# Performance work log

Hardware: AMD Instinct MI355X
Metric: run time of the kernel (lower is better)

## Reference

```python
import jax, jax.numpy as jnp
import numpy as np

NP_, NG_ = 20000, 5000            # protein / go_annotation node counts
D_FEAT, D_HID, N_CLS = 512, 128, 1000
E_PP, E_PG, E_GP = 240000, 100000, 100000
NEG_SLOPE = -0.2                  # note: the repo default slope is negative
EPS = 1e-12


def _l2norm(x):
    n = jnp.linalg.norm(x, axis=1, keepdims=True)
    return x / jnp.maximum(n, EPS)


def _edge_softmax(logits, dst, n):
    # per-destination-node softmax over incoming edges, per feature channel
    m = jax.ops.segment_max(logits, dst, num_segments=n)
    e = jnp.exp(logits - m[dst])
    s = jax.ops.segment_sum(e, dst, num_segments=n)
    return e / s[dst]


def _type_attn(h_src, h_dst, src, dst, Wl, bl, Wr, br):
    # GCN-normalized aggregation onto dst nodes, then type-level attention logits,
    # broadcast back to edges (copy_u on the reversed relation graph).
    ns, nd = h_src.shape[0], h_dst.shape[0]
    ones = jnp.ones(src.shape[0], dtype=h_src.dtype)
    outdeg = jnp.clip(jax.ops.segment_sum(ones, src, num_segments=ns), 1.0)
    feat = h_src * (outdeg ** -0.5)[:, None]
    rst = jax.ops.segment_sum(feat[src], dst, num_segments=nd)
    indeg = jnp.clip(jax.ops.segment_sum(ones, dst, num_segments=nd), 1.0)
    rst = rst * (indeg ** -0.5)[:, None]
    ea = jax.nn.elu((h_dst @ Wl + bl) + (rst @ Wr + br))  # [nd, D_HID]
    return ea[dst]                                        # [E, D_HID]


def setup_inputs() -> dict:
    key = jax.random.key(0)
    ks = iter(jax.random.split(key, 40))

    def nrm(shape, s=0.05):
        return jax.random.normal(next(ks), shape, dtype=jnp.float32) * s

    def ri(n, hi):
        return jax.random.randint(next(ks), (n,), 0, hi, dtype=jnp.int32)

    zeros = lambda n: jnp.zeros((n,), jnp.float32)
    return dict(
        x_protein=jax.random.normal(next(ks), (NP_, D_FEAT), dtype=jnp.float32),
        x_go=jax.random.normal(next(ks), (NG_, N_CLS), dtype=jnp.float32),
        src_pp=ri(E_PP, NP_), dst_pp=ri(E_PP, NP_),
        src_pg=ri(E_PG, NP_), dst_pg=ri(E_PG, NG_),
        src_gp=ri(E_GP, NG_), dst_gp=ri(E_GP, NP_),
        W1p=nrm((D_FEAT, D_HID)), b1p=zeros(D_HID),
        W1g=nrm((N_CLS, D_HID)), b1g=zeros(D_HID),
        Wl_p=nrm((D_HID, D_HID)), bl_p=zeros(D_HID),
        Wl_g=nrm((D_HID, D_HID)), bl_g=zeros(D_HID),
        Wr_p=nrm((D_HID, D_HID)), br_p=zeros(D_HID),
        Wr_g=nrm((D_HID, D_HID)), br_g=zeros(D_HID),
        Wnl=nrm((D_HID, D_HID)), bnl=zeros(D_HID),
        Wnr=nrm((D_HID, D_HID)), bnr=zeros(D_HID),
        Wfc=nrm((D_HID, N_CLS)), bfc=zeros(N_CLS),
    )


def reference(x_protein, x_go, src_pp, dst_pp, src_pg, dst_pg, src_gp, dst_gp,
              W1p, b1p, W1g, b1g, Wl_p, bl_p, Wl_g, bl_g,
              Wr_p, br_p, Wr_g, br_g, Wnl, bnl, Wnr, bnr, Wfc, bfc):
    # input projection + row-wise l2 norm (dropout disabled / eval mode)
    hp = _l2norm(x_protein @ W1p + b1p)   # [NP, D_HID]
    hg = _l2norm(x_go @ W1g + b1g)        # [NG, D_HID]

    # ---- TypeAttention over each canonical etype ----
    a_pp = _type_attn(hp, hp, src_pp, dst_pp, Wl_p, bl_p, Wr_p, br_p)
    a_pg = _type_attn(hp, hg, src_pg, dst_pg, Wl_g, bl_g, Wr_p, br_p)
    a_gp = _type_attn(hg, hp, src_gp, dst_gp, Wl_p, bl_p, Wr_g, br_g)

    # homogeneous view: proteins [0,NP), go_annotation [NP,NP+NG)
    gsrc = jnp.concatenate([src_pp, src_pg, src_gp + NP_])
    gdst = jnp.concatenate([dst_pp, dst_pg + NP_, dst_gp])
    alpha = jnp.concatenate([a_pp, a_pg, a_gp], axis=0)   # [E, D_HID]
    n = NP_ + NG_
    alpha = _edge_softmax(alpha, gdst, n)

    # ---- NodeAttention on the homogeneous graph ----
    x = jnp.concatenate([hp, hg], axis=0)                 # [N, D_HID]
    hl = (x @ Wnl + bnl)[gsrc]
    hr = (x @ Wnr + bnr)[gdst]
    e = (hl + hr) * alpha
    e = jnp.where(e > 0, e, NEG_SLOPE * e)                # LeakyReLU(slope=-0.2)
    a = _edge_softmax(e, gdst, n)
    h = jax.ops.segment_sum(x[gsrc] * a, gdst, num_segments=n)

    out = h @ Wfc + bfc   # [N, N_CLS]; rows [:NP]=protein, [NP:]=go_annotation
    return out
```

## Files before the change

kernel.cpp:

```cpp
#include <hip/hip_runtime.h>
#include <math.h>

#define NP 20000
#define NG 5000
#define NTOT 25000
#define DF 512
#define NCLS 1000
#define DH 128
#define EPP 240000
#define EPG 100000
#define EGP 100000
#define ETOT 440000
#define FS 16
#define HB 16

typedef __attribute__((ext_vector_type(8))) __bf16 bf16x8;
typedef __attribute__((ext_vector_type(4))) float f32x4;

__device__ __forceinline__ void gl2lds16(const void* g, void* l) {
    __builtin_amdgcn_global_load_lds(
        (const __attribute__((address_space(1))) unsigned int*)g,
        (__attribute__((address_space(3))) unsigned int*)l, 16, 0, 0);
}

__device__ __forceinline__ float b2f(unsigned short u) {
    union { unsigned int i; float f; } c; c.i = ((unsigned int)u) << 16; return c.f;
}

__global__ __launch_bounds__(1024) void hist_part_kernel(
    const int* __restrict__ src_pp, const int* __restrict__ dst_pp,
    const int* __restrict__ src_pg, const int* __restrict__ dst_pg,
    const int* __restrict__ src_gp, const int* __restrict__ dst_gp,
    int* __restrict__ partial)
{
    __shared__ int bins[20000];
    const int job = blockIdx.y, b = blockIdx.x;
    const int* idx; int nbins, nedge; size_t pbase;
    switch (job) {
    case 0: idx = src_pp; nbins = 20000; nedge = EPP; pbase = 0;       break;
    case 1: idx = dst_pp; nbins = 20000; nedge = EPP; pbase = 320000;  break;
    case 2: idx = src_pg; nbins = 20000; nedge = EPG; pbase = 640000;  break;
    case 3: idx = dst_pg; nbins = 5000;  nedge = EPG; pbase = 960000;  break;
    case 4: idx = src_gp; nbins = 5000;  nedge = EGP; pbase = 1040000; break;
    default: idx = dst_gp; nbins = 20000; nedge = EGP; pbase = 1120000; break;
    }
    for (int i = threadIdx.x; i < nbins; i += 1024) bins[i] = 0;
    __syncthreads();
    const int chunk = (nedge + HB - 1) / HB;
    const int e0 = b * chunk, e1 = min(e0 + chunk, nedge);
    for (int e = e0 + threadIdx.x; e < e1; e += 1024) atomicAdd(&bins[idx[e]], 1);
    __syncthreads();
    int* dst = partial + pbase + (size_t)b * nbins;
    for (int i = threadIdx.x; i < nbins; i += 1024) dst[i] = bins[i];
}

__global__ __launch_bounds__(256) void hist_merge_kernel(const int* __restrict__ partial,
    int* __restrict__ outdeg_pp, int* __restrict__ indeg_pp,
    int* __restrict__ outdeg_pg, int* __restrict__ indeg_pg,
    int* __restrict__ outdeg_gp, int* __restrict__ indeg_gp)
{
    const int job = blockIdx.y;
    const int nbins = (job == 3 || job == 4) ? 5000 : 20000;
    const int bin = blockIdx.x * 256 + threadIdx.x;
    if (bin >= nbins) return;
    size_t pbase;
    int* outp;
    switch (job) {
    case 0: pbase = 0;       outp = outdeg_pp; break;
    case 1: pbase = 320000;  outp = indeg_pp;  break;
    case 2: pbase = 640000;  outp = outdeg_pg; break;
    case 3: pbase = 960000;  outp = indeg_pg;  break;
    case 4: pbase = 1040000; outp = outdeg_gp; break;
    default: pbase = 1120000; outp = indeg_gp; break;
    }
    const int* p = partial + pbase + bin;
    int s = 0;
#pragma unroll
    for (int b = 0; b < HB; b++) s += p[(size_t)b * nbins];
    outp[bin] = s;
}

__global__ __launch_bounds__(1024) void scan_kernel(const int* __restrict__ indeg_pp,
                                                    const int* __restrict__ indeg_gp,
                                                    const int* __restrict__ indeg_pg,
                                                    int* __restrict__ row_ptr)
{
    __shared__ int part[1024];
    int t = threadIdx.x;
    const int CH = (NTOT + 1023) / 1024;
    int base = t * CH;
    auto cntf = [&](int idx) -> int {
        return (idx < NP) ? (indeg_pp[idx] + indeg_gp[idx]) : indeg_pg[idx - NP];
    };
    int s = 0;
    for (int i = 0; i < CH; i++) { int idx = base + i; if (idx < NTOT) s += cntf(idx); }
    part[t] = s;
    __syncthreads();
    for (int off = 1; off < 1024; off <<= 1) {
        int v = (t >= off) ? part[t - off] : 0;
        __syncthreads();
        part[t] += v;
        __syncthreads();
    }
    int run = (t == 0) ? 0 : part[t - 1];
    for (int i = 0; i < CH; i++) {
        int idx = base + i;
        if (idx < NTOT) { row_ptr[idx] = run; run += cntf(idx); }
    }
    if (t == 1023) row_ptr[NTOT] = part[1023];
}

__global__ void scatter_kernel(const int* __restrict__ src_pp, const int* __restrict__ dst_pp,
                               const int* __restrict__ src_pg, const int* __restrict__ dst_pg,
                               const int* __restrict__ src_gp, const int* __restrict__ dst_gp,
                               const int* __restrict__ outdeg_pp, const int* __restrict__ outdeg_pg,
                               const int* __restrict__ outdeg_gp,
                               const int* __restrict__ row_ptr, int* fill,
                               int2* __restrict__ edata)
{
    int e = blockIdx.x * blockDim.x + threadIdx.x;
    int s, d, t; float sc;
    if (e < EPP) {
        s = src_pp[e]; d = dst_pp[e]; t = 0;
        sc = rsqrtf((float)max(outdeg_pp[s], 1));
    } else if (e < EPP + EPG) {
        int i = e - EPP; s = src_pg[i]; d = NP + dst_pg[i]; t = 1;
        sc = rsqrtf((float)max(outdeg_pg[s], 1));
    } else if (e < ETOT) {
        int i = e - EPP - EPG; int sl = src_gp[i]; s = NP + sl; d = dst_gp[i]; t = 2;
        sc = rsqrtf((float)max(outdeg_gp[sl], 1));
    } else return;
    int pos = row_ptr[d] + atomicAdd(&fill[d * FS], 1);
    edata[pos] = make_int2(s | (t << 16), __float_as_int(sc));
}

__global__ __launch_bounds__(256) void conv_x_kernel(const float* __restrict__ xp, const float* __restrict__ xg,
                                                     __bf16* __restrict__ xpb, __bf16* __restrict__ xgb)
{
    long long e = ((long long)blockIdx.x * 256 + threadIdx.x) * 8;
    __bf16 pk[8];
    if (blockIdx.y == 0) {
        if (e >= (long long)20032 * 512) return;
        int row = (int)(e >> 9), k = (int)(e & 511);
        if (row < NP) {
            f32x4 v0 = *(const f32x4*)(xp + (size_t)row * 512 + k);
            f32x4 v1 = *(const f32x4*)(xp + (size_t)row * 512 + k + 4);
#pragma unroll
            for (int i = 0; i < 4; i++) { pk[i] = (__bf16)v0[i]; pk[4 + i] = (__bf16)v1[i]; }
        } else {
#pragma unroll
            for (int i = 0; i < 8; i++) pk[i] = (__bf16)0.f;
        }
        *(bf16x8*)(xpb + e) = *(bf16x8*)pk;
    } else {
        if (e >= (long long)5056 * 1024) return;
        int row = (int)(e >> 10), k = (int)(e & 1023);
        if (row < NG && k + 7 < 1000) {
            f32x4 v0 = *(const f32x4*)(xg + (size_t)row * 1000 + k);
            f32x4 v1 = *(const f32x4*)(xg + (size_t)row * 1000 + k + 4);
#pragma unroll
            for (int i = 0; i < 4; i++) { pk[i] = (__bf16)v0[i]; pk[4 + i] = (__bf16)v1[i]; }
        } else {
#pragma unroll
            for (int i = 0; i < 8; i++) {
                int kk = k + i;
                pk[i] = (__bf16)((row < NG && kk < 1000) ? xg[(size_t)row * 1000 + kk] : 0.f);
            }
        }
        *(bf16x8*)(xgb + e) = *(bf16x8*)pk;
    }
}

__global__ __launch_bounds__(256) void conv_w_kernel(
    const float* W1p, const float* W1g, const float* Wlp, const float* Wrp, const float* Wrg,
    const float* Wnl, const float* Wnr, const float* Wfc,
    __bf16* w1pt, __bf16* w1gt, __bf16* wlpt, __bf16* wrpt, __bf16* wrgt,
    __bf16* wnlt, __bf16* wnrt, __bf16* wfct)
{
    int e = blockIdx.x * 256 + threadIdx.x;
    switch (blockIdx.y) {
    case 0: if (e < 128 * 512)  { int n = e >> 9, k = e & 511;  w1pt[e] = (__bf16)W1p[(size_t)k * 128 + n]; } break;
    case 1: if (e < 128 * 1024) { int n = e >> 10, k = e & 1023; w1gt[e] = (__bf16)(k < 1000 ? W1g[(size_t)k * 128 + n] : 0.f); } break;
    case 2: if (e < 16384) { int n = e >> 7, k = e & 127; wlpt[e] = (__bf16)Wlp[(size_t)k * 128 + n]; } break;
    case 3: if (e < 16384) { int n = e >> 7, k = e & 127; wrpt[e] = (__bf16)Wrp[(size_t)k * 128 + n]; } break;
    case 4: if (e < 16384) { int n = e >> 7, k = e & 127; wrgt[e] = (__bf16)Wrg[(size_t)k * 128 + n]; } break;
    case 5: if (e < 16384) { int n = e >> 7, k = e & 127; wnlt[e] = (__bf16)Wnl[(size_t)k * 128 + n]; } break;
    case 6: if (e < 16384) { int n = e >> 7, k = e & 127; wnrt[e] = (__bf16)Wnr[(size_t)k * 128 + n]; } break;
    case 7: if (e < 1024 * 128) { int n = e >> 7, k = e & 127; wfct[e] = (__bf16)(n < 1000 ? Wfc[(size_t)k * 1000 + n] : 0.f); } break;
    }
}

struct GJob {
    const __bf16* A1; const __bf16* A2;
    const __bf16* B1; const __bf16* B2;
    const float* b1; const float* b2;
    float* O1; float* O2; __bf16* Ob;
    int M, N, Kp, ksteps;
};

template<int ACT, int DUALA, int DUALW, int EMIT>
__global__ __launch_bounds__(256) void gemm_bt(GJob j0, GJob j1, int split)
{
    __shared__ __align__(16) __bf16 As[64 * 32];
    __shared__ __align__(16) __bf16 A2s[DUALA ? 64 * 32 : 8];
    __shared__ __align__(16) __bf16 Bs[128 * 32];
    __shared__ __align__(16) __bf16 B2s[(DUALA || DUALW) ? 128 * 32 : 8];
    __shared__ float part[2][64];

    GJob j; int bx;
    if ((int)blockIdx.x < split) { j = j0; bx = blockIdx.x; }
    else { j = j1; bx = blockIdx.x - split; }

    const int tid = threadIdx.x;
    const int wave = tid >> 6, lane = tid & 63;
    const int wr = wave >> 1, wc = wave & 1;
    const int l15 = lane & 15, lh = lane >> 4;
    const int row0 = bx * 64;
    const int col0 = blockIdx.y * 128;

    const size_t aoff = (size_t)(row0 + (tid >> 2)) * j.Kp + (tid & 3) * 8;
    const size_t boff0 = (size_t)(col0 + (tid >> 2)) * j.Kp + (tid & 3) * 8;
    const size_t boff1 = boff0 + (size_t)64 * j.Kp;
    char* alds  = (char*)As + wave * 1024;
    char* a2lds = (char*)A2s + wave * 1024;
    char* blds0 = (char*)Bs + wave * 1024;
    char* blds1 = (char*)Bs + 4096 + wave * 1024;
    char* b2lds0 = (char*)B2s + wave * 1024;
    char* b2lds1 = (char*)B2s + 4096 + wave * 1024;

    f32x4 acc[2][4], acc2[2][4];
#pragma unroll
    for (int fm = 0; fm < 2; fm++)
#pragma unroll
        for (int fn = 0; fn < 4; fn++) {
            acc[fm][fn] = (f32x4)0.f;
            if (DUALW) acc2[fm][fn] = (f32x4)0.f;
        }

    for (int ks = 0; ks < j.ksteps; ks++) {
        const int k0 = ks * 32;
        __syncthreads();
        gl2lds16(j.A1 + aoff + k0, alds);
        if (DUALA) gl2lds16(j.A2 + aoff + k0, a2lds);
        gl2lds16(j.B1 + boff0 + k0, blds0);
        gl2lds16(j.B1 + boff1 + k0, blds1);
        if (DUALA || DUALW) {
            gl2lds16(j.B2 + boff0 + k0, b2lds0);
            gl2lds16(j.B2 + boff1 + k0, b2lds1);
        }
        __syncthreads();

#pragma unroll
        for (int fm = 0; fm < 2; fm++) {
            bf16x8 a = *(const bf16x8*)&As[(wr * 32 + fm * 16 + l15) * 32 + lh * 8];
            bf16x8 a2;
            if (DUALA) a2 = *(const bf16x8*)&A2s[(wr * 32 + fm * 16 + l15) * 32 + lh * 8];
#pragma unroll
            for (int fn = 0; fn < 4; fn++) {
                bf16x8 b = *(const bf16x8*)&Bs[(wc * 64 + fn * 16 + l15) * 32 + lh * 8];
                acc[fm][fn] = __builtin_amdgcn_mfma_f32_16x16x32_bf16(a, b, acc[fm][fn], 0, 0, 0);
                if (DUALA) {
                    bf16x8 b2 = *(const bf16x8*)&B2s[(wc * 64 + fn * 16 + l15) * 32 + lh * 8];
                    acc[fm][fn] = __builtin_amdgcn_mfma_f32_16x16x32_bf16(a2, b2, acc[fm][fn], 0, 0, 0);
                }
                if (DUALW) {
                    bf16x8 b2 = *(const bf16x8*)&B2s[(wc * 64 + fn * 16 + l15) * 32 + lh * 8];
                    acc2[fm][fn] = __builtin_amdgcn_mfma_f32_16x16x32_bf16(a, b2, acc2[fm][fn], 0, 0, 0);
                }
            }
        }
    }

    float bias[4], bias2[4];
#pragma unroll
    for (int fn = 0; fn < 4; fn++) {
        int col = col0 + wc * 64 + fn * 16 + l15;
        bias[fn] = 0.f; bias2[fn] = 0.f;
        if (col < j.N) {
            bias[fn] = DUALA ? (j.b1[col] + j.b2[col]) : j.b1[col];
            if (DUALW) bias2[fn] = j.b2[col];
        }
    }

    float vv[2][4][4];
#pragma unroll
    for (int fm = 0; fm < 2; fm++)
#pragma unroll
        for (int fn = 0; fn < 4; fn++)
#pragma unroll
            for (int r = 0; r < 4; r++) {
                float v = acc[fm][fn][r] + bias[fn];
                if (ACT == 1) v = v > 0.f ? v : (expf(v) - 1.f);
                vv[fm][fn][r] = v;
            }

    float scale[2][4];
#pragma unroll
    for (int fm = 0; fm < 2; fm++)
#pragma unroll
        for (int r = 0; r < 4; r++) scale[fm][r] = 1.f;

    if (ACT == 2) {
        float s[2][4];
#pragma unroll
        for (int fm = 0; fm < 2; fm++)
#pragma unroll
            for (int r = 0; r < 4; r++) {
                float v = 0.f;
#pragma unroll
                for (int fn = 0; fn < 4; fn++) v += vv[fm][fn][r] * vv[fm][fn][r];
                v += __shfl_xor(v, 1);
                v += __shfl_xor(v, 2);
                v += __shfl_xor(v, 4);
                v += __shfl_xor(v, 8);
                s[fm][r] = v;
            }
        __syncthreads();
        if (l15 == 0) {
#pragma unroll
            for (int fm = 0; fm < 2; fm++)
#pragma unroll
                for (int r = 0; r < 4; r++)
                    part[wc][wr * 32 + fm * 16 + lh * 4 + r] = s[fm][r];
        }
        __syncthreads();
#pragma unroll
        for (int fm = 0; fm < 2; fm++)
#pragma unroll
            for (int r = 0; r < 4; r++) {
                int rl = wr * 32 + fm * 16 + lh * 4 + r;
                float ss = part[0][rl] + part[1][rl];
                scale[fm][r] = 1.f / fmaxf(sqrtf(ss), 1e-12f);
            }
    }

#pragma unroll
    for (int fm = 0; fm < 2; fm++)
#pragma unroll
        for (int fn = 0; fn < 4; fn++)
#pragma unroll
            for (int r = 0; r < 4; r++) {
                int row = row0 + wr * 32 + fm * 16 + lh * 4 + r;
                int col = col0 + wc * 64 + fn * 16 + l15;
                if (row < j.M && col < j.N) {
                    float v = vv[fm][fn][r] * scale[fm][r];
                    if (EMIT != 2) j.O1[(size_t)row * j.N + col] = v;
                    if (EMIT != 0) j.Ob[(size_t)row * j.N + col] = (__bf16)v;
                    if (DUALW) j.O2[(size_t)row * j.N + col] = acc2[fm][fn][r] + bias2[fn];
                }
            }
}

__global__ __launch_bounds__(128) void rst_agg_kernel(const __bf16* __restrict__ x,
                                                      const int* __restrict__ row_ptr,
                                                      const int2* __restrict__ edata,
                                                      const int* __restrict__ indeg_pp,
                                                      const int* __restrict__ indeg_gp,
                                                      __bf16* __restrict__ rppb, __bf16* __restrict__ rgpb)
{
    int d = blockIdx.x;
    int c = threadIdx.x;
    int beg = row_ptr[d], end = row_ptr[d + 1];
    float spp = 0.f, sgp = 0.f;
    __shared__ int pl[128];
    __shared__ float sc[128];
    const unsigned short* xu = (const unsigned short*)x;
    for (int base = beg; base < end; base += 128) {
        int n = min(128, end - base);
        __syncthreads();
        if (c < n) { int2 e2 = edata[base + c]; pl[c] = e2.x; sc[c] = __int_as_float(e2.y); }
        __syncthreads();
        for (int i = 0; i < n; i++) {
            int p = pl[i]; int s = p & 0xFFFF; int t = p >> 16;
            float v = b2f(xu[(size_t)s * DH + c]) * sc[i];
            if (t == 0) spp += v; else sgp += v;
        }
    }
    float ipp = rsqrtf((float)max(indeg_pp[d], 1));
    float igp = rsqrtf((float)max(indeg_gp[d], 1));
    rppb[(size_t)d * DH + c] = (__bf16)(spp * ipp);
    rgpb[(size_t)d * DH + c] = (__bf16)(sgp * igp);
}

__global__ void wa_kernel(const int* __restrict__ indeg_pp, const int* __restrict__ indeg_gp,
                          float* __restrict__ eapp, float* __restrict__ eagp)
{
    int idx = blockIdx.x * blockDim.x + threadIdx.x;
    if (idx >= NP * DH) return;
    int d = idx >> 7;
    int npp = indeg_pp[d], ngp = indeg_gp[d];
    float app = eapp[idx], agp = eagp[idx];
    float wpp = 0.f, wgp = 0.f;
    if (npp > 0 && ngp > 0) {
        float mx = fmaxf(app, agp);
        float epp = __expf(app - mx), egp = __expf(agp - mx);
        float den = (float)npp * epp + (float)ngp * egp;
        wpp = epp / den; wgp = egp / den;
    } else if (npp > 0) wpp = 1.f / (float)npp;
    else if (ngp > 0) wgp = 1.f / (float)ngp;
    eapp[idx] = wpp;
    eagp[idx] = wgp;
}

__global__ __launch_bounds__(128) void node_attn_kernel(const __bf16* __restrict__ x,
                                                        const __bf16* __restrict__ hlb,
                                                        const float* __restrict__ hr,
                                                        const float* __restrict__ wpp_arr, const float* __restrict__ wgp_arr,
                                                        const int* __restrict__ indeg_pg,
                                                        const int* __restrict__ row_ptr, const int2* __restrict__ edata,
                                                        __bf16* __restrict__ hb)
{
    int d = blockIdx.x, c = threadIdx.x;
    int beg = row_ptr[d], end = row_ptr[d + 1];
    float hrd = hr[(size_t)d * DH + c];
    float wpp = 0.f, wgp = 0.f;
    if (d < NP) {
        wpp = wpp_arr[(size_t)d * DH + c];
        wgp = wgp_arr[(size_t)d * DH + c];
    } else {
        float wpg = 1.f / (float)max(indeg_pg[d - NP], 1);
        wpp = wpg; wgp = wpg;
    }
    float ssum = 0.f, acc = 0.f;
    __shared__ int pl[128];
    const unsigned short* xu = (const unsigned short*)x;
    const unsigned short* hu = (const unsigned short*)hlb;
    for (int base = beg; base < end; base += 128) {
        int n = min(128, end - base);
        __syncthreads();
        if (c < n) pl[c] = edata[base + c].x;
        __syncthreads();
        for (int i = 0; i < n; i++) {
            int p = pl[i]; int s = p & 0xFFFF; int t = p >> 16;
            float al = (t == 0) ? wpp : wgp;
            float e = (b2f(hu[(size_t)s * DH + c]) + hrd) * al;
            e = fmaxf(e, -0.2f * e);
            float pw = __expf(e);
            float xv = b2f(xu[(size_t)s * DH + c]);
            ssum += pw;
            acc += pw * xv;
        }
    }
    hb[(size_t)d * DH + c] = (__bf16)((end > beg) ? acc / ssum : 0.f);
}

extern "C" void kernel_launch(void* const* d_in, const int* in_sizes, int n_in,
                              void* d_out, int out_size, void* d_ws, size_t ws_size,
                              hipStream_t stream)
{
    const float* x_protein = (const float*)d_in[0];
    const float* x_go      = (const float*)d_in[1];
    const int* src_pp = (const int*)d_in[2];
    const int* dst_pp = (const int*)d_in[3];
    const int* src_pg = (const int*)d_in[4];
    const int* dst_pg = (const int*)d_in[5];
    const int* src_gp = (const int*)d_in[6];
    const int* dst_gp = (const int*)d_in[7];
    const float* W1p = (const float*)d_in[8];
    const float* b1p = (const float*)d_in[9];
    const float* W1g = (const float*)d_in[10];
    const float* b1g = (const float*)d_in[11];
    const float* Wl_p = (const float*)d_in[12];
    const float* bl_p = (const float*)d_in[13];
    const float* Wr_p = (const float*)d_in[16];
    const float* br_p = (const float*)d_in[17];
    const float* Wr_g = (const float*)d_in[18];
    const float* br_g = (const float*)d_in[19];
    const float* Wnl = (const float*)d_in[20];
    const float* bnl = (const float*)d_in[21];
    const float* Wnr = (const float*)d_in[22];
    const float* bnr = (const float*)d_in[23];
    const float* Wfc = (const float*)d_in[24];
    const float* bfc = (const float*)d_in[25];
    float* out = (float*)d_out;

    size_t off = 0;
    char* base = (char*)d_ws;
    auto alloc = [&](size_t words) { void* p = base + off * 4; off += (words + 7) & ~(size_t)7; return p; };

    __bf16* xb   = (__bf16*)alloc((size_t)25024 * 128 / 2);
    float*  hr   = (float*)alloc((size_t)25000 * 128);
    __bf16* hlb  = (__bf16*)alloc((size_t)25024 * 128 / 2);
    __bf16* rppb = (__bf16*)alloc((size_t)20032 * 128 / 2);
    __bf16* rgpb = (__bf16*)alloc((size_t)20032 * 128 / 2);
    char* R1 = (char*)alloc((size_t)5128192 + 2588672);
    int*    partial = (int*)R1;
    __bf16* xpb = (__bf16*)R1;
    __bf16* xgb = (__bf16*)(R1 + (size_t)20032 * 512 * 2);
    float*  wpp = (float*)R1;
    float*  wgp = wpp + (size_t)20000 * 128;
    __bf16* haggb = (__bf16*)(wgp + (size_t)20000 * 128);
    __bf16* w1pt = (__bf16*)alloc(128 * 512 / 2);
    __bf16* w1gt = (__bf16*)alloc(128 * 1024 / 2);
    __bf16* wlpt = (__bf16*)alloc(128 * 128 / 2);
    __bf16* wrpt = (__bf16*)alloc(128 * 128 / 2);
    __bf16* wrgt = (__bf16*)alloc(128 * 128 / 2);
    __bf16* wnlt = (__bf16*)alloc(128 * 128 / 2);
    __bf16* wnrt = (__bf16*)alloc(128 * 128 / 2);
    __bf16* wfct = (__bf16*)alloc(1024 * 128 / 2);
    int* outdeg_pp = (int*)alloc(NP);
    int* outdeg_pg = (int*)alloc(NP);
    int* outdeg_gp = (int*)alloc(NG);
    int* indeg_pp  = (int*)alloc(NP);
    int* indeg_gp  = (int*)alloc(NP);
    int* indeg_pg  = (int*)alloc(NG);
    int* fill      = (int*)alloc((size_t)NTOT * FS);
    int* row_ptr   = (int*)alloc(NTOT + 1);
    int2* edata    = (int2*)alloc((size_t)ETOT * 2);

    hipMemsetAsync(fill, 0, (size_t)NTOT * FS * sizeof(int), stream);

    hist_part_kernel<<<dim3(HB, 6), 1024, 0, stream>>>(
        src_pp, dst_pp, src_pg, dst_pg, src_gp, dst_gp, partial);
    hist_merge_kernel<<<dim3((20000 + 255) / 256, 6), 256, 0, stream>>>(
        partial, outdeg_pp, indeg_pp, outdeg_pg, indeg_pg, outdeg_gp, indeg_gp);
    scan_kernel<<<1, 1024, 0, stream>>>(indeg_pp, indeg_gp, indeg_pg, row_ptr);
    scatter_kernel<<<(ETOT + 255) / 256, 256, 0, stream>>>(
        src_pp, dst_pp, src_pg, dst_pg, src_gp, dst_gp,
        outdeg_pp, outdeg_pg, outdeg_gp, row_ptr, fill, edata);

    conv_x_kernel<<<dim3(5008, 2), 256, 0, stream>>>(x_protein, x_go, xpb, xgb);
    conv_w_kernel<<<dim3(512, 8), 256, 0, stream>>>(W1p, W1g, Wl_p, Wr_p, Wr_g, Wnl, Wnr, Wfc,
                                                    w1pt, w1gt, wlpt, wrpt, wrgt, wnlt, wnrt, wfct);

    {
        GJob p0 = { xpb, nullptr, w1pt, nullptr, b1p, nullptr, nullptr, nullptr, xb, NP, 128, 512, 16 };
        GJob p1 = { xgb, nullptr, w1gt, nullptr, b1g, nullptr, nullptr, nullptr,
                    xb + (size_t)NP * 128, NG, 128, 1024, 32 };
        gemm_bt<2, 0, 0, 2><<<392, 256, 0, stream>>>(p0, p1, 313);
    }

    rst_agg_kernel<<<NP, 128, 0, stream>>>(xb, row_ptr, edata, indeg_pp, indeg_gp, rppb, rgpb);

    {
        GJob e0 = { xb, rppb, wlpt, wrpt, bl_p, br_p, wpp, nullptr, nullptr, NP, 128, 128, 4 };
        GJob e1 = { xb, rgpb, wlpt, wrgt, bl_p, br_g, wgp, nullptr, nullptr, NP, 128, 128, 4 };
        gemm_bt<1, 1, 0, 0><<<626, 256, 0, stream>>>(e0, e1, 313);
    }

    wa_kernel<<<(NP * DH + 255) / 256, 256, 0, stream>>>(indeg_pp, indeg_gp, wpp, wgp);

    {
        GJob h0 = { xb, nullptr, wnlt, wnrt, bnl, bnr, nullptr, hr, hlb, NTOT, 128, 128, 4 };
        gemm_bt<0, 0, 1, 2><<<391, 256, 0, stream>>>(h0, h0, 1 << 30);
    }

    node_attn_kernel<<<NTOT, 128, 0, stream>>>(xb, hlb, hr, wpp, wgp, indeg_pg, row_ptr, edata, haggb);

    {
        GJob o0 = { haggb, nullptr, wfct, nullptr, bfc, nullptr, out, nullptr, nullptr, NTOT, NCLS, 128, 4 };
        gemm_bt<0, 0, 0, 0><<<dim3(391, 8), 256, 0, stream>>>(o0, o0, 1 << 30);
    }

    (void)in_sizes; (void)n_in; (void)out_size; (void)ws_size;
}
```

Before: 264.3 us.

## Fuse fp32 protein conversion into GEMM, merge type-attn GEMM with softmax, interleave x/hl

The protein feature matrix is now loaded in fp32 straight into the projection GEMM and converted to bf16 in registers, so the separate conversion pass and its bf16 buffer go away. The two type-attention GEMMs and the weight-softmax kernel become one kernel that computes the three products and the ELU and softmax in its epilogue. x and hl are stored interleaved so node attention reads both with one 32-bit load, and hr is now stored in bf16. Both gather kernels move to 256 threads, with the edges split between two halves and combined through LDS. In exchange, hr loses precision and the fp32 A tile doubles the LDS traffic of the projection GEMM.

```diff
diff --git a/kernel.cpp b/kernel.cpp
--- a/kernel.cpp
+++ b/kernel.cpp
@@ -11,7 +11,7 @@
 #define EPG 100000
 #define EGP 100000
 #define ETOT 440000
-#define FS 16
+#define FS 8
 #define HB 16
 
 typedef __attribute__((ext_vector_type(8))) __bf16 bf16x8;
@@ -63,8 +63,7 @@
     const int nbins = (job == 3 || job == 4) ? 5000 : 20000;
     const int bin = blockIdx.x * 256 + threadIdx.x;
     if (bin >= nbins) return;
-    size_t pbase;
-    int* outp;
+    size_t pbase; int* outp;
     switch (job) {
     case 0: pbase = 0;       outp = outdeg_pp; break;
     case 1: pbase = 320000;  outp = indeg_pp;  break;
@@ -134,41 +133,25 @@
     edata[pos] = make_int2(s | (t << 16), __float_as_int(sc));
 }
 
-__global__ __launch_bounds__(256) void conv_x_kernel(const float* __restrict__ xp, const float* __restrict__ xg,
-                                                     __bf16* __restrict__ xpb, __bf16* __restrict__ xgb)
+__global__ __launch_bounds__(256) void conv_xg_kernel(const float* __restrict__ xg, __bf16* __restrict__ xgb)
 {
     long long e = ((long long)blockIdx.x * 256 + threadIdx.x) * 8;
+    if (e >= (long long)5056 * 1024) return;
+    int row = (int)(e >> 10), k = (int)(e & 1023);
     __bf16 pk[8];
-    if (blockIdx.y == 0) {
-        if (e >= (long long)20032 * 512) return;
-        int row = (int)(e >> 9), k = (int)(e & 511);
-        if (row < NP) {
-            f32x4 v0 = *(const f32x4*)(xp + (size_t)row * 512 + k);
-            f32x4 v1 = *(const f32x4*)(xp + (size_t)row * 512 + k + 4);
-#pragma unroll
-            for (int i = 0; i < 4; i++) { pk[i] = (__bf16)v0[i]; pk[4 + i] = (__bf16)v1[i]; }
-        } else {
-#pragma unroll
-            for (int i = 0; i < 8; i++) pk[i] = (__bf16)0.f;
-        }
-        *(bf16x8*)(xpb + e) = *(bf16x8*)pk;
+    if (row < NG && k + 7 < 1000) {
+        f32x4 v0 = *(const f32x4*)(xg + (size_t)row * 1000 + k);
+        f32x4 v1 = *(const f32x4*)(xg + (size_t)row * 1000 + k + 4);
+#pragma unroll
+        for (int i = 0; i < 4; i++) { pk[i] = (__bf16)v0[i]; pk[4 + i] = (__bf16)v1[i]; }
     } else {
-        if (e >= (long long)5056 * 1024) return;
-        int row = (int)(e >> 10), k = (int)(e & 1023);
-        if (row < NG && k + 7 < 1000) {
-            f32x4 v0 = *(const f32x4*)(xg + (size_t)row * 1000 + k);
-            f32x4 v1 = *(const f32x4*)(xg + (size_t)row * 1000 + k + 4);
-#pragma unroll
-            for (int i = 0; i < 4; i++) { pk[i] = (__bf16)v0[i]; pk[4 + i] = (__bf16)v1[i]; }
-        } else {
-#pragma unroll
-            for (int i = 0; i < 8; i++) {
-                int kk = k + i;
-                pk[i] = (__bf16)((row < NG && kk < 1000) ? xg[(size_t)row * 1000 + kk] : 0.f);
-            }
-        }
-        *(bf16x8*)(xgb + e) = *(bf16x8*)pk;
-    }
+#pragma unroll
+        for (int i = 0; i < 8; i++) {
+            int kk = k + i;
+            pk[i] = (__bf16)((row < NG && kk < 1000) ? xg[(size_t)row * 1000 + kk] : 0.f);
+        }
+    }
+    *(bf16x8*)(xgb + e) = *(bf16x8*)pk;
 }
 
 __global__ __launch_bounds__(256) void conv_w_kernel(
@@ -191,40 +174,41 @@
 }
 
 struct GJob {
-    const __bf16* A1; const __bf16* A2;
-    const __bf16* B1; const __bf16* B2;
+    const void* A1; const __bf16* B1; const __bf16* B2;
     const float* b1; const float* b2;
-    float* O1; float* O2; __bf16* Ob;
+    float* O1; void* O2; __bf16* Ob; __bf16* Oi;
     int M, N, Kp, ksteps;
 };
 
-template<int ACT, int DUALA, int DUALW, int EMIT>
-__global__ __launch_bounds__(256) void gemm_bt(GJob j0, GJob j1, int split)
-{
-    __shared__ __align__(16) __bf16 As[64 * 32];
-    __shared__ __align__(16) __bf16 A2s[DUALA ? 64 * 32 : 8];
+template<int ACT, int DUALW, int EMIT, int AF32>
+__global__ __launch_bounds__(256) void gemm_bt(GJob j)
+{
+    __shared__ __align__(16) __bf16 As[AF32 ? 8 : 64 * 32];
+    __shared__ __align__(16) float Asf[AF32 ? 64 * 32 : 4];
     __shared__ __align__(16) __bf16 Bs[128 * 32];
-    __shared__ __align__(16) __bf16 B2s[(DUALA || DUALW) ? 128 * 32 : 8];
+    __shared__ __align__(16) __bf16 B2s[DUALW ? 128 * 32 : 8];
     __shared__ float part[2][64];
-
-    GJob j; int bx;
-    if ((int)blockIdx.x < split) { j = j0; bx = blockIdx.x; }
-    else { j = j1; bx = blockIdx.x - split; }
 
     const int tid = threadIdx.x;
     const int wave = tid >> 6, lane = tid & 63;
     const int wr = wave >> 1, wc = wave & 1;
     const int l15 = lane & 15, lh = lane >> 4;
-    const int row0 = bx * 64;
+    const int row0 = blockIdx.x * 64;
     const int col0 = blockIdx.y * 128;
 
+    const __bf16* A1b = (const __bf16*)j.A1;
+    const float*  A1f = (const float*)j.A1;
+
     const size_t aoff = (size_t)(row0 + (tid >> 2)) * j.Kp + (tid & 3) * 8;
+    const size_t a0off = (size_t)min(row0 + (tid >> 3), j.M - 1) * j.Kp + (tid & 7) * 4;
+    const size_t a1off = (size_t)min(row0 + 32 + (tid >> 3), j.M - 1) * j.Kp + (tid & 7) * 4;
     const size_t boff0 = (size_t)(col0 + (tid >> 2)) * j.Kp + (tid & 3) * 8;
     const size_t boff1 = boff0 + (size_t)64 * j.Kp;
-    char* alds  = (char*)As + wave * 1024;
-    char* a2lds = (char*)A2s + wave * 1024;
-    char* blds0 = (char*)Bs + wave * 1024;
-    char* blds1 = (char*)Bs + 4096 + wave * 1024;
+    char* alds   = (char*)As + wave * 1024;
+    char* aldsf0 = (char*)Asf + wave * 1024;
+    char* aldsf1 = (char*)Asf + 4096 + wave * 1024;
+    char* blds0  = (char*)Bs + wave * 1024;
+    char* blds1  = (char*)Bs + 4096 + wave * 1024;
     char* b2lds0 = (char*)B2s + wave * 1024;
     char* b2lds1 = (char*)B2s + 4096 + wave * 1024;
 
@@ -240,11 +224,15 @@
     for (int ks = 0; ks < j.ksteps; ks++) {
         const int k0 = ks * 32;
         __syncthreads();
-        gl2lds16(j.A1 + aoff + k0, alds);
-        if (DUALA) gl2lds16(j.A2 + aoff + k0, a2lds);
+        if constexpr (AF32) {
+            gl2lds16(A1f + a0off + k0, aldsf0);
+            gl2lds16(A1f + a1off + k0, aldsf1);
+        } else {
+            gl2lds16(A1b + aoff + k0, alds);
+        }
         gl2lds16(j.B1 + boff0 + k0, blds0);
         gl2lds16(j.B1 + boff1 + k0, blds1);
-        if (DUALA || DUALW) {
+        if constexpr (DUALW) {
             gl2lds16(j.B2 + boff0 + k0, b2lds0);
             gl2lds16(j.B2 + boff1 + k0, b2lds1);
         }
@@ -252,18 +240,23 @@
 
 #pragma unroll
         for (int fm = 0; fm < 2; fm++) {
-            bf16x8 a = *(const bf16x8*)&As[(wr * 32 + fm * 16 + l15) * 32 + lh * 8];
-            bf16x8 a2;
-            if (DUALA) a2 = *(const bf16x8*)&A2s[(wr * 32 + fm * 16 + l15) * 32 + lh * 8];
+            bf16x8 a;
+            if constexpr (AF32) {
+                const float* ap = &Asf[(wr * 32 + fm * 16 + l15) * 32 + lh * 8];
+                f32x4 a0 = *(const f32x4*)ap;
+                f32x4 a1 = *(const f32x4*)(ap + 4);
+                __bf16 pk[8];
+#pragma unroll
+                for (int i = 0; i < 4; i++) { pk[i] = (__bf16)a0[i]; pk[4 + i] = (__bf16)a1[i]; }
+                a = *(bf16x8*)pk;
+            } else {
+                a = *(const bf16x8*)&As[(wr * 32 + fm * 16 + l15) * 32 + lh * 8];
+            }
 #pragma unroll
             for (int fn = 0; fn < 4; fn++) {
                 bf16x8 b = *(const bf16x8*)&Bs[(wc * 64 + fn * 16 + l15) * 32 + lh * 8];
                 acc[fm][fn] = __builtin_amdgcn_mfma_f32_16x16x32_bf16(a, b, acc[fm][fn], 0, 0, 0);
-                if (DUALA) {
-                    bf16x8 b2 = *(const bf16x8*)&B2s[(wc * 64 + fn * 16 + l15) * 32 + lh * 8];
-                    acc[fm][fn] = __builtin_amdgcn_mfma_f32_16x16x32_bf16(a2, b2, acc[fm][fn], 0, 0, 0);
-                }
-                if (DUALW) {
+                if constexpr (DUALW) {
                     bf16x8 b2 = *(const bf16x8*)&B2s[(wc * 64 + fn * 16 + l15) * 32 + lh * 8];
                     acc2[fm][fn] = __builtin_amdgcn_mfma_f32_16x16x32_bf16(a, b2, acc2[fm][fn], 0, 0, 0);
                 }
@@ -277,7 +270,7 @@
         int col = col0 + wc * 64 + fn * 16 + l15;
         bias[fn] = 0.f; bias2[fn] = 0.f;
         if (col < j.N) {
-            bias[fn] = DUALA ? (j.b1[col] + j.b2[col]) : j.b1[col];
+            bias[fn] = j.b1[col];
             if (DUALW) bias2[fn] = j.b2[col];
         }
     }
@@ -288,11 +281,7 @@
 #pragma unroll
         for (int fn = 0; fn < 4; fn++)
 #pragma unroll
-            for (int r = 0; r < 4; r++) {
-                float v = acc[fm][fn][r] + bias[fn];
-                if (ACT == 1) v = v > 0.f ? v : (expf(v) - 1.f);
-                vv[fm][fn][r] = v;
-            }
+            for (int r = 0; r < 4; r++) vv[fm][fn][r] = acc[fm][fn][r] + bias[fn];
 
     float scale[2][4];
 #pragma unroll
@@ -300,7 +289,7 @@
 #pragma unroll
         for (int r = 0; r < 4; r++) scale[fm][r] = 1.f;
 
-    if (ACT == 2) {
+    if constexpr (ACT == 2) {
         float s[2][4];
 #pragma unroll
         for (int fm = 0; fm < 2; fm++)
@@ -344,14 +333,122 @@
                 int col = col0 + wc * 64 + fn * 16 + l15;
                 if (row < j.M && col < j.N) {
                     float v = vv[fm][fn][r] * scale[fm][r];
-                    if (EMIT != 2) j.O1[(size_t)row * j.N + col] = v;
-                    if (EMIT != 0) j.Ob[(size_t)row * j.N + col] = (__bf16)v;
-                    if (DUALW) j.O2[(size_t)row * j.N + col] = acc2[fm][fn][r] + bias2[fn];
+                    if constexpr (EMIT == 0) j.O1[(size_t)row * j.N + col] = v;
+                    if constexpr (EMIT == 2) j.Ob[(size_t)row * j.N + col] = (__bf16)v;
+                    if constexpr (EMIT == 3) {
+                        j.Ob[(size_t)row * j.N + col] = (__bf16)v;
+                        j.Oi[(size_t)row * 256 + col * 2] = (__bf16)v;
+                    }
+                    if constexpr (EMIT == 4) j.Oi[(size_t)row * 256 + col * 2 + 1] = (__bf16)v;
+                    if constexpr (DUALW)
+                        ((__bf16*)j.O2)[(size_t)row * j.N + col] = (__bf16)(acc2[fm][fn][r] + bias2[fn]);
                 }
             }
 }
 
-__global__ __launch_bounds__(128) void rst_agg_kernel(const __bf16* __restrict__ x,
+__global__ __launch_bounds__(256) void ea_wa_kernel(
+    const __bf16* __restrict__ xb, const __bf16* __restrict__ rppb, const __bf16* __restrict__ rgpb,
+    const __bf16* __restrict__ wl, const __bf16* __restrict__ wrp, const __bf16* __restrict__ wrg,
+    const float* __restrict__ blp, const float* __restrict__ brp, const float* __restrict__ brg,
+    const int* __restrict__ indeg_pp, const int* __restrict__ indeg_gp,
+    float* __restrict__ wpp, float* __restrict__ wgp)
+{
+    __shared__ __align__(16) __bf16 A1s[64 * 32], A2s[64 * 32], A3s[64 * 32];
+    __shared__ __align__(16) __bf16 B1s[128 * 32], B2s[128 * 32], B3s[128 * 32];
+
+    const int tid = threadIdx.x;
+    const int wave = tid >> 6, lane = tid & 63;
+    const int wr = wave >> 1, wc = wave & 1;
+    const int l15 = lane & 15, lh = lane >> 4;
+    const int row0 = blockIdx.x * 64;
+
+    const size_t aoff = (size_t)(row0 + (tid >> 2)) * 128 + (tid & 3) * 8;
+    const size_t boff0 = (size_t)(tid >> 2) * 128 + (tid & 3) * 8;
+    const size_t boff1 = boff0 + (size_t)64 * 128;
+    char* a1 = (char*)A1s + wave * 1024;
+    char* a2 = (char*)A2s + wave * 1024;
+    char* a3 = (char*)A3s + wave * 1024;
+    char* b1l0 = (char*)B1s + wave * 1024, *b1l1 = (char*)B1s + 4096 + wave * 1024;
+    char* b2l0 = (char*)B2s + wave * 1024, *b2l1 = (char*)B2s + 4096 + wave * 1024;
+    char* b3l0 = (char*)B3s + wave * 1024, *b3l1 = (char*)B3s + 4096 + wave * 1024;
+
+    f32x4 accL[2][4], accP[2][4], accG[2][4];
+#pragma unroll
+    for (int fm = 0; fm < 2; fm++)
+#pragma unroll
+        for (int fn = 0; fn < 4; fn++) {
+            accL[fm][fn] = (f32x4)0.f; accP[fm][fn] = (f32x4)0.f; accG[fm][fn] = (f32x4)0.f;
+        }
+
+    for (int ks = 0; ks < 4; ks++) {
+        const int k0 = ks * 32;
+        __syncthreads();
+        gl2lds16(xb + aoff + k0, a1);
+        gl2lds16(rppb + aoff + k0, a2);
+        gl2lds16(rgpb + aoff + k0, a3);
+        gl2lds16(wl + boff0 + k0, b1l0);  gl2lds16(wl + boff1 + k0, b1l1);
+        gl2lds16(wrp + boff0 + k0, b2l0); gl2lds16(wrp + boff1 + k0, b2l1);
+        gl2lds16(wrg + boff0 + k0, b3l0); gl2lds16(wrg + boff1 + k0, b3l1);
+        __syncthreads();
+
+#pragma unroll
+        for (int fm = 0; fm < 2; fm++) {
+            const int arow = (wr * 32 + fm * 16 + l15) * 32 + lh * 8;
+            bf16x8 aL = *(const bf16x8*)&A1s[arow];
+            bf16x8 aP = *(const bf16x8*)&A2s[arow];
+            bf16x8 aG = *(const bf16x8*)&A3s[arow];
+#pragma unroll
+            for (int fn = 0; fn < 4; fn++) {
+                const int brow = (wc * 64 + fn * 16 + l15) * 32 + lh * 8;
+                bf16x8 bL = *(const bf16x8*)&B1s[brow];
+                bf16x8 bP = *(const bf16x8*)&B2s[brow];
+                bf16x8 bG = *(const bf16x8*)&B3s[brow];
+                accL[fm][fn] = __builtin_amdgcn_mfma_f32_16x16x32_bf16(aL, bL, accL[fm][fn], 0, 0, 0);
+                accP[fm][fn] = __builtin_amdgcn_mfma_f32_16x16x32_bf16(aP, bP, accP[fm][fn], 0, 0, 0);
+                accG[fm][fn] = __builtin_amdgcn_mfma_f32_16x16x32_bf16(aG, bG, accG[fm][fn], 0, 0, 0);
+            }
+        }
+    }
+
+    float bp[4], bg[4];
+#pragma unroll
+    for (int fn = 0; fn < 4; fn++) {
+        int col = wc * 64 + fn * 16 + l15;
+        bp[fn] = blp[col] + brp[col];
+        bg[fn] = blp[col] + brg[col];
+    }
+
+#pragma unroll
+    for (int fm = 0; fm < 2; fm++)
+#pragma unroll
+        for (int r = 0; r < 4; r++) {
+            int row = row0 + wr * 32 + fm * 16 + lh * 4 + r;
+            int rr = min(row, NP - 1);
+            int npp = indeg_pp[rr], ngp = indeg_gp[rr];
+#pragma unroll
+            for (int fn = 0; fn < 4; fn++) {
+                int col = wc * 64 + fn * 16 + l15;
+                float app = accL[fm][fn][r] + accP[fm][fn][r] + bp[fn];
+                app = app > 0.f ? app : (__expf(app) - 1.f);
+                float agp = accL[fm][fn][r] + accG[fm][fn][r] + bg[fn];
+                agp = agp > 0.f ? agp : (__expf(agp) - 1.f);
+                float wppv = 0.f, wgpv = 0.f;
+                if (npp > 0 && ngp > 0) {
+                    float mx = fmaxf(app, agp);
+                    float ep = __expf(app - mx), eg = __expf(agp - mx);
+                    float den = (float)npp * ep + (float)ngp * eg;
+                    wppv = ep / den; wgpv = eg / den;
+                } else if (npp > 0) wppv = 1.f / (float)npp;
+                else if (ngp > 0) wgpv = 1.f / (float)ngp;
+                if (row < NP) {
+                    wpp[(size_t)row * DH + col] = wppv;
+                    wgp[(size_t)row * DH + col] = wgpv;
+                }
+            }
+        }
+}
+
+__global__ __launch_bounds__(256) void rst_agg_kernel(const __bf16* __restrict__ x,
                                                       const int* __restrict__ row_ptr,
                                                       const int2* __restrict__ edata,
                                                       const int* __restrict__ indeg_pp,
@@ -359,89 +456,86 @@
                                                       __bf16* __restrict__ rppb, __bf16* __restrict__ rgpb)
 {
     int d = blockIdx.x;
-    int c = threadIdx.x;
+    int tid = threadIdx.x;
+    int c = tid & 127, h = tid >> 7;
     int beg = row_ptr[d], end = row_ptr[d + 1];
     float spp = 0.f, sgp = 0.f;
     __shared__ int pl[128];
     __shared__ float sc[128];
+    __shared__ float red[2][2][128];
     const unsigned short* xu = (const unsigned short*)x;
     for (int base = beg; base < end; base += 128) {
         int n = min(128, end - base);
         __syncthreads();
-        if (c < n) { int2 e2 = edata[base + c]; pl[c] = e2.x; sc[c] = __int_as_float(e2.y); }
-        __syncthreads();
-        for (int i = 0; i < n; i++) {
+        if (tid < n) { int2 e2 = edata[base + tid]; pl[tid] = e2.x; sc[tid] = __int_as_float(e2.y); }
+        __syncthreads();
+        for (int i = h; i < n; i += 2) {
             int p = pl[i]; int s = p & 0xFFFF; int t = p >> 16;
             float v = b2f(xu[(size_t)s * DH + c]) * sc[i];
             if (t == 0) spp += v; else sgp += v;
         }
     }
-    float ipp = rsqrtf((float)max(indeg_pp[d], 1));
-    float igp = rsqrtf((float)max(indeg_gp[d], 1));
-    rppb[(size_t)d * DH + c] = (__bf16)(spp * ipp);
-    rgpb[(size_t)d * DH + c] = (__bf16)(sgp * igp);
-}
-
-__global__ void wa_kernel(const int* __restrict__ indeg_pp, const int* __restrict__ indeg_gp,
-                          float* __restrict__ eapp, float* __restrict__ eagp)
-{
-    int idx = blockIdx.x * blockDim.x + threadIdx.x;
-    if (idx >= NP * DH) return;
-    int d = idx >> 7;
-    int npp = indeg_pp[d], ngp = indeg_gp[d];
-    float app = eapp[idx], agp = eagp[idx];
-    float wpp = 0.f, wgp = 0.f;
-    if (npp > 0 && ngp > 0) {
-        float mx = fmaxf(app, agp);
-        float epp = __expf(app - mx), egp = __expf(agp - mx);
-        float den = (float)npp * epp + (float)ngp * egp;
-        wpp = epp / den; wgp = egp / den;
-    } else if (npp > 0) wpp = 1.f / (float)npp;
-    else if (ngp > 0) wgp = 1.f / (float)ngp;
-    eapp[idx] = wpp;
-    eagp[idx] = wgp;
-}
-
-__global__ __launch_bounds__(128) void node_attn_kernel(const __bf16* __restrict__ x,
-                                                        const __bf16* __restrict__ hlb,
-                                                        const float* __restrict__ hr,
+    red[h][0][c] = spp; red[h][1][c] = sgp;
+    __syncthreads();
+    if (h == 0) {
+        float tp = spp + red[1][0][c];
+        float tg = sgp + red[1][1][c];
+        float ipp = rsqrtf((float)max(indeg_pp[d], 1));
+        float igp = rsqrtf((float)max(indeg_gp[d], 1));
+        rppb[(size_t)d * DH + c] = (__bf16)(tp * ipp);
+        rgpb[(size_t)d * DH + c] = (__bf16)(tg * igp);
+    }
+}
+
+__global__ __launch_bounds__(256) void node_attn_kernel(const __bf16* __restrict__ xhl,
+                                                        const __bf16* __restrict__ hrb,
                                                         const float* __restrict__ wpp_arr, const float* __restrict__ wgp_arr,
                                                         const int* __restrict__ indeg_pg,
                                                         const int* __restrict__ row_ptr, const int2* __restrict__ edata,
                                                         __bf16* __restrict__ hb)
 {
-    int d = blockIdx.x, c = threadIdx.x;
+    int d = blockIdx.x;
+    int tid = threadIdx.x;
+    int c = tid & 127, h = tid >> 7;
     int beg = row_ptr[d], end = row_ptr[d + 1];
-    float hrd = hr[(size_t)d * DH + c];
-    float wpp = 0.f, wgp = 0.f;
+    float hrd = b2f(((const unsigned short*)hrb)[(size_t)d * DH + c]);
+    float wppv, wgpv;
     if (d < NP) {
-        wpp = wpp_arr[(size_t)d * DH + c];
-        wgp = wgp_arr[(size_t)d * DH + c];
+        wppv = wpp_arr[(size_t)d * DH + c];
+        wgpv = wgp_arr[(size_t)d * DH + c];
     } else {
-        float wpg = 1.f / (float)max(indeg_pg[d - NP], 1);
-        wpp = wpg; wgp = wpg;
+        float w = 1.f / (float)max(indeg_pg[d - NP], 1);
+        wppv = w; wgpv = w;
     }
     float ssum = 0.f, acc = 0.f;
     __shared__ int pl[128];
-    const unsigned short* xu = (const unsigned short*)x;
-    const unsigned short* hu = (const unsigned short*)hlb;
+    __shared__ float red[2][2][128];
+    const unsigned int* xu = (const unsigned int*)xhl;
     for (int base = beg; base < end; base += 128) {
         int n = min(128, end - base);
         __syncthreads();
-        if (c < n) pl[c] = edata[base + c].x;
-        __syncthreads();
-        for (int i = 0; i < n; i++) {
+        if (tid < n) pl[tid] = edata[base + tid].x;
+        __syncthreads();
+        for (int i = h; i < n; i += 2) {
             int p = pl[i]; int s = p & 0xFFFF; int t = p >> 16;
-            float al = (t == 0) ? wpp : wgp;
-            float e = (b2f(hu[(size_t)s * DH + c]) + hrd) * al;
+            unsigned int u = xu[(size_t)s * 128 + c];
+            float xv  = b2f((unsigned short)(u & 0xFFFFu));
+            float hlv = b2f((unsigned short)(u >> 16));
+            float al = (t == 0) ? wppv : wgpv;
+            float e = (hlv + hrd) * al;
             e = fmaxf(e, -0.2f * e);
             float pw = __expf(e);
-            float xv = b2f(xu[(size_t)s * DH + c]);
             ssum += pw;
             acc += pw * xv;
         }
     }
-    hb[(size_t)d * DH + c] = (__bf16)((end > beg) ? acc / ssum : 0.f);
+    red[h][0][c] = ssum; red[h][1][c] = acc;
+    __syncthreads();
+    if (h == 0) {
+        float ts = ssum + red[1][0][c];
+        float ta = acc + red[1][1][c];
+        hb[(size_t)d * DH + c] = (__bf16)((end > beg) ? ta / ts : 0.f);
+    }
 }
 
 extern "C" void kernel_launch(void* const* d_in, const int* in_sizes, int n_in,
@@ -479,14 +573,13 @@
     auto alloc = [&](size_t words) { void* p = base + off * 4; off += (words + 7) & ~(size_t)7; return p; };
 
     __bf16* xb   = (__bf16*)alloc((size_t)25024 * 128 / 2);
-    float*  hr   = (float*)alloc((size_t)25000 * 128);
-    __bf16* hlb  = (__bf16*)alloc((size_t)25024 * 128 / 2);
+    __bf16* xhl  = (__bf16*)alloc((size_t)25024 * 256 / 2);
+    __bf16* hrb  = (__bf16*)alloc((size_t)25024 * 128 / 2);
     __bf16* rppb = (__bf16*)alloc((size_t)20032 * 128 / 2);
     __bf16* rgpb = (__bf16*)alloc((size_t)20032 * 128 / 2);
-    char* R1 = (char*)alloc((size_t)5128192 + 2588672);
+    char* R1 = (char*)alloc(6722000);
     int*    partial = (int*)R1;
-    __bf16* xpb = (__bf16*)R1;
-    __bf16* xgb = (__bf16*)(R1 + (size_t)20032 * 512 * 2);
+    __bf16* xgb = (__bf16*)R1;
     float*  wpp = (float*)R1;
     float*  wgp = wpp + (size_t)20000 * 128;
     __bf16* haggb = (__bf16*)(wgp + (size_t)20000 * 128);
@@ -519,37 +612,35 @@
         src_pp, dst_pp, src_pg, dst_pg, src_gp, dst_gp,
         outdeg_pp, outdeg_pg, outdeg_gp, row_ptr, fill, edata);
 
-    conv_x_kernel<<<dim3(5008, 2), 256, 0, stream>>>(x_protein, x_go, xpb, xgb);
+    conv_xg_kernel<<<2528, 256, 0, stream>>>(x_go, xgb);
     conv_w_kernel<<<dim3(512, 8), 256, 0, stream>>>(W1p, W1g, Wl_p, Wr_p, Wr_g, Wnl, Wnr, Wfc,
                                                     w1pt, w1gt, wlpt, wrpt, wrgt, wnlt, wnrt, wfct);
 
     {
-        GJob p0 = { xpb, nullptr, w1pt, nullptr, b1p, nullptr, nullptr, nullptr, xb, NP, 128, 512, 16 };
-        GJob p1 = { xgb, nullptr, w1gt, nullptr, b1g, nullptr, nullptr, nullptr,
-                    xb + (size_t)NP * 128, NG, 128, 1024, 32 };
-        gemm_bt<2, 0, 0, 2><<<392, 256, 0, stream>>>(p0, p1, 313);
-    }
-
-    rst_agg_kernel<<<NP, 128, 0, stream>>>(xb, row_ptr, edata, indeg_pp, indeg_gp, rppb, rgpb);
-
+        GJob p = { x_protein, w1pt, nullptr, b1p, nullptr, nullptr, nullptr, xb, xhl, NP, 128, 512, 16 };
+        gemm_bt<2, 0, 3, 1><<<313, 256, 0, stream>>>(p);
+    }
     {
-        GJob e0 = { xb, rppb, wlpt, wrpt, bl_p, br_p, wpp, nullptr, nullptr, NP, 128, 128, 4 };
-        GJob e1 = { xb, rgpb, wlpt, wrgt, bl_p, br_g, wgp, nullptr, nullptr, NP, 128, 128, 4 };
-        gemm_bt<1, 1, 0, 0><<<626, 256, 0, stream>>>(e0, e1, 313);
-    }
-
-    wa_kernel<<<(NP * DH + 255) / 256, 256, 0, stream>>>(indeg_pp, indeg_gp, wpp, wgp);
+        GJob p = { xgb, w1gt, nullptr, b1g, nullptr, nullptr, nullptr,
+                   xb + (size_t)NP * 128, xhl + (size_t)NP * 256, NG, 128, 1024, 32 };
+        gemm_bt<2, 0, 3, 0><<<79, 256, 0, stream>>>(p);
+    }
+
+    rst_agg_kernel<<<NP, 256, 0, stream>>>(xb, row_ptr, edata, indeg_pp, indeg_gp, rppb, rgpb);
+
+    ea_wa_kernel<<<313, 256, 0, stream>>>(xb, rppb, rgpb, wlpt, wrpt, wrgt,
+                                          bl_p, br_p, br_g, indeg_pp, indeg_gp, wpp, wgp);
 
     {
-        GJob h0 = { xb, nullptr, wnlt, wnrt, bnl, bnr, nullptr, hr, hlb, NTOT, 128, 128, 4 };
-        gemm_bt<0, 0, 1, 2><<<391, 256, 0, stream>>>(h0, h0, 1 << 30);
-    }
-
-    node_attn_kernel<<<NTOT, 128, 0, stream>>>(xb, hlb, hr, wpp, wgp, indeg_pg, row_ptr, edata, haggb);
+        GJob h0 = { xb, wnlt, wnrt, bnl, bnr, nullptr, hrb, nullptr, xhl, NTOT, 128, 128, 4 };
+        gemm_bt<0, 1, 4, 0><<<391, 256, 0, stream>>>(h0);
+    }
+
+    node_attn_kernel<<<NTOT, 256, 0, stream>>>(xhl, hrb, wpp, wgp, indeg_pg, row_ptr, edata, haggb);
 
     {
-        GJob o0 = { haggb, nullptr, wfct, nullptr, bfc, nullptr, out, nullptr, nullptr, NTOT, NCLS, 128, 4 };
-        gemm_bt<0, 0, 0, 0><<<dim3(391, 8), 256, 0, stream>>>(o0, o0, 1 << 30);
+        GJob o0 = { haggb, wfct, nullptr, bfc, nullptr, out, nullptr, nullptr, nullptr, NTOT, NCLS, 128, 4 };
+        gemm_bt<0, 0, 0, 0><<<dim3(391, 8), 256, 0, stream>>>(o0);
     }
 
     (void)in_sizes; (void)n_in; (void)out_size; (void)ws_size;
```

Result: slower. 327.2 us (+23.8%).
